# Kernel tuning notes

Hardware: AMD Instinct MI355X
Metric: run time of the kernel (lower is better)

## Reference

```python
import jax, jax.numpy as jnp
import numpy as np

TOKEN_SELF_ATTN_VALUE = -50000.0


def setup_inputs() -> dict:
    key = jax.random.key(0)
    k1, k2, k3 = jax.random.split(key, 3)
    batch, seqlen, dim = 16, 4096, 64
    n_hashes, bucket_size = 8, 64
    n_buckets = seqlen // bucket_size  # 64
    qk = jax.random.normal(k1, (batch, seqlen, dim), dtype=jnp.float32)
    v = jax.random.normal(k2, (batch, seqlen, dim), dtype=jnp.float32)
    # random rotations for LSH hashing: (dim, n_hashes, n_buckets // 2)
    rotations = jax.random.normal(k3, (dim, n_hashes, n_buckets // 2), dtype=jnp.float32)
    return {"qk": qk, "v": v, "rotations": rotations}


def reference(qk, v, rotations):
    batch, seqlen, dim = qk.shape
    n_hashes = rotations.shape[1]
    n_buckets = 2 * rotations.shape[2]
    bucket_size = seqlen // n_buckets

    # ---- hash_vectors (rehash_each_round=True, no hash dropout) ----
    rotated = jnp.einsum('btf,fhi->bhti', qk, rotations)       # (b, h, t, nb/2)
    rotated = jnp.concatenate([rotated, -rotated], axis=-1)    # (b, h, t, nb)
    buckets = jnp.argmax(rotated, axis=-1)                     # (b, h, t)
    offsets = (jnp.arange(n_hashes) * n_buckets)[None, :, None]
    buckets = (buckets + offsets).reshape(batch, n_hashes * seqlen)

    # ---- sort tokens by (bucket, position) ----
    ticker = jnp.arange(n_hashes * seqlen)
    buckets_and_t = seqlen * buckets + (ticker % seqlen)[None, :]
    sticker = jnp.argsort(buckets_and_t, axis=-1)              # keys are unique
    undo_sort = jnp.argsort(sticker, axis=-1)
    st = sticker % seqlen                                      # original positions

    sqk = jnp.take_along_axis(qk, st[:, :, None], axis=1)      # (b, h*t, d)
    sv = jnp.take_along_axis(v, st[:, :, None], axis=1)

    chunk_size = n_hashes * n_buckets
    bq_t = st.reshape(batch, chunk_size, bucket_size)
    bqk = sqk.reshape(batch, chunk_size, bucket_size, dim)
    bv = sv.reshape(batch, chunk_size, bucket_size, dim)

    bq = bqk
    # F.normalize(p=2, eps=1e-12)
    bk = bqk / jnp.maximum(jnp.linalg.norm(bqk, axis=-1, keepdims=True), 1e-12)

    def look_one_back(x):
        return jnp.concatenate([x, jnp.roll(x, 1, axis=1)], axis=2)

    bk = look_one_back(bk)
    bv = look_one_back(bv)
    bkv_t = look_one_back(bq_t)

    dots = jnp.einsum('bcie,bcje->bcij', bq, bk) * (dim ** -0.5)  # (b, chunks, i, 2i)

    # self-attention mask (causal=False, no input masks by default)
    self_mask = bq_t[:, :, :, None] == bkv_t[:, :, None, :]
    dots = jnp.where(self_mask, TOKEN_SELF_ATTN_VALUE, dots)

    dots_logsumexp = jax.scipy.special.logsumexp(dots, axis=-1, keepdims=True)
    probs = jnp.exp(dots - dots_logsumexp)
    bo = jnp.einsum('bcij,bcje->bcie', probs, bv)

    so = bo.reshape(batch, -1, dim)                   # (b, h*t, d)
    slogits = dots_logsumexp.reshape(batch, -1)       # (b, h*t)

    # unsort back to original token order
    o = jnp.take_along_axis(so, undo_sort[:, :, None], axis=1)
    logits = jnp.take_along_axis(slogits, undo_sort, axis=1)

    o = o.reshape(batch, n_hashes, seqlen, dim)
    logits = logits.reshape(batch, n_hashes, seqlen, 1)

    # combine hash rounds weighted by their logsumexps
    w = jnp.exp(logits - jax.scipy.special.logsumexp(logits, axis=1, keepdims=True))
    out = jnp.sum(o * w, axis=1)                      # (b, t, d)
    return out
```

## Files before the change

### kernel.cpp

```cpp
#include <hip/hip_runtime.h>

#define BATCH  16
#define SEQ    4096
#define DIM    64
#define NHASH  8
#define NCHUNK 512
#define SB     72

typedef __attribute__((ext_vector_type(8))) short short8;
typedef __attribute__((ext_vector_type(4))) float floatx4;

__device__ __forceinline__ float trunc_hi(float a) {
    return __uint_as_float(__float_as_uint(a) & 0xffff0000u);
}
__device__ __forceinline__ unsigned pack_hi2(float a, float b) {
    return (__float_as_uint(a) >> 16) | (__float_as_uint(b) & 0xffff0000u);
}
__device__ __forceinline__ void hi16_store(const float* xs, short* dst) {
    unsigned hd[8];
#pragma unroll
    for (int u = 0; u < 8; ++u) hd[u] = pack_hi2(xs[2*u], xs[2*u + 1]);
    *(uint4*)(dst)     = make_uint4(hd[0], hd[1], hd[2], hd[3]);
    *(uint4*)(dst + 8) = make_uint4(hd[4], hd[5], hd[6], hd[7]);
}
__device__ __forceinline__ void split8_frag(const float* xs, short8* hi, short8* lo) {
    union { unsigned u[4]; short8 s; } H, L;
#pragma unroll
    for (int u = 0; u < 4; ++u) {
        float a = xs[2*u], b = xs[2*u + 1];
        H.u[u] = pack_hi2(a, b);
        L.u[u] = pack_hi2(a - trunc_hi(a), b - trunc_hi(b));
    }
    *hi = H.s; *lo = L.s;
}

__global__ __launch_bounds__(256, 2) void lsh_hash_kernel(
    const float* __restrict__ qk, const float* __restrict__ rot,
    int* __restrict__ buckets)
{
    __shared__ float rs[64 * 128];
    int tid = threadIdx.x;
    int tb   = blockIdx.x >> 1;
    int hsel = blockIdx.x & 1;

    {
        const float4* rg = (const float4*)rot;
#pragma unroll
        for (int j = 0; j < 8; ++j) {
            int idx4 = j * 256 + tid;
            int f = idx4 >> 5, r4 = idx4 & 31;
            ((float4*)rs)[idx4] = rg[f * 64 + hsel * 32 + r4];
        }
    }
    __syncthreads();

    int tt = tid & 127;
    int hh = tid >> 7;
    int gid0 = tb * 256 + tt;
    int gid1 = gid0 + 128;
    const float* q0 = qk + (size_t)gid0 * DIM;
    const float* q1 = qk + (size_t)gid1 * DIM;

#pragma unroll
    for (int h0 = 0; h0 < 2; ++h0) {
        int hp = hh * 2 + h0;
        const float* rbase = rs + hp * 32;
        float a0[32], a1[32];
#pragma unroll
        for (int i = 0; i < 32; ++i) { a0[i] = 0.f; a1[i] = 0.f; }
#pragma unroll 1
        for (int ft = 0; ft < 8; ++ft) {
            float qa[8], qb[8];
            *(float4*)&qa[0] = *(const float4*)(q0 + ft * 8);
            *(float4*)&qa[4] = *(const float4*)(q0 + ft * 8 + 4);
            *(float4*)&qb[0] = *(const float4*)(q1 + ft * 8);
            *(float4*)&qb[4] = *(const float4*)(q1 + ft * 8 + 4);
#pragma unroll
            for (int f8 = 0; f8 < 8; ++f8) {
                const float* rp = rbase + (ft * 8 + f8) * 128;
                float x = qa[f8], y = qb[f8];
#pragma unroll
                for (int i = 0; i < 32; ++i) {
                    float r = rp[i];
                    a0[i] = fmaf(x, r, a0[i]);
                    a1[i] = fmaf(y, r, a1[i]);
                }
            }
        }
        int h = hsel * 4 + hp;
        {
            float best = a0[0]; int bi = 0;
#pragma unroll
            for (int i = 1; i < 32; ++i) { if (a0[i] > best) { best = a0[i]; bi = i; } }
#pragma unroll
            for (int i = 0; i < 32; ++i) { float nv = -a0[i]; if (nv > best) { best = nv; bi = i + 32; } }
            int b = gid0 >> 12, t = gid0 & 4095;
            buckets[((size_t)b * NHASH + h) * SEQ + t] = bi;
        }
        {
            float best = a1[0]; int bi = 0;
#pragma unroll
            for (int i = 1; i < 32; ++i) { if (a1[i] > best) { best = a1[i]; bi = i; } }
#pragma unroll
            for (int i = 0; i < 32; ++i) { float nv = -a1[i]; if (nv > best) { best = nv; bi = i + 32; } }
            int b = gid1 >> 12, t = gid1 & 4095;
            buckets[((size_t)b * NHASH + h) * SEQ + t] = bi;
        }
    }
}

__global__ __launch_bounds__(256) void lsh_sort_kernel(
    const int* __restrict__ buckets, int* __restrict__ st)
{
    __shared__ int hist[256 * 65];
    __shared__ int seg[256];
    __shared__ int base[64];

    int bh = blockIdx.x;
    int tid = threadIdx.x;
    int w = tid >> 6, lane = tid & 63;

    for (int i = tid; i < 256 * 65; i += 256) hist[i] = 0;

    int myb[16];
    {
        const int4* bp4 = (const int4*)(buckets + (size_t)bh * SEQ);
#pragma unroll
        for (int u4 = 0; u4 < 4; ++u4) {
            int4 bb = bp4[tid * 4 + u4];
            myb[u4*4+0] = bb.x; myb[u4*4+1] = bb.y;
            myb[u4*4+2] = bb.z; myb[u4*4+3] = bb.w;
        }
    }
    __syncthreads();
    int* hrow = &hist[tid * 65];
#pragma unroll
    for (int u = 0; u < 16; ++u) hrow[myb[u]] += 1;
    __syncthreads();

    {
        int run = 0;
        for (int tp = 0; tp < 64; ++tp) {
            int idx = (w * 64 + tp) * 65 + lane;
            int c0 = hist[idx];
            hist[idx] = run;
            run += c0;
        }
        seg[w * 64 + lane] = run;
    }
    __syncthreads();
    if (tid < 64) {
        int s0 = seg[lane], s1 = seg[64 + lane], s2 = seg[128 + lane], s3 = seg[192 + lane];
        seg[lane] = 0; seg[64 + lane] = s0;
        seg[128 + lane] = s0 + s1; seg[192 + lane] = s0 + s1 + s2;
        int tot = s0 + s1 + s2 + s3;
        int x = tot;
#pragma unroll
        for (int d = 1; d < 64; d <<= 1) {
            int y = __shfl_up(x, d, 64);
            if (lane >= d) x += y;
        }
        base[lane] = x - tot;
    }
    __syncthreads();

    int* op = st + (size_t)bh * SEQ;
#pragma unroll
    for (int u = 0; u < 16; ++u) {
        int bb = myb[u];
        int local = hrow[bb];
        hrow[bb] = local + 1;
        int pos = base[bb] + seg[w * 64 + bb] + local;
        op[pos] = tid * 16 + u;
    }
}

__global__ __launch_bounds__(256, 5) void lsh_attn_kernel(
    const float* __restrict__ qk, const float* __restrict__ v,
    const int* __restrict__ st, float* __restrict__ Obuf, float* __restrict__ Dbuf)
{
    __shared__ short Khi[64 * SB];
    __shared__ short Psp[64 * SB];
    __shared__ short Vhi[64 * SB];
    __shared__ int   tk[64];

    short* Phi = Khi;
    short* Plo = Psp;

    int tid  = threadIdx.x;
    int lane = tid & 63;
    int w    = tid >> 6;
    int quad = lane >> 4;
    int l15  = lane & 15;

    int bc = blockIdx.x;
    int b = bc >> 9, c = bc & (NCHUNK - 1);
    int cm = (c + NCHUNK - 1) & (NCHUNK - 1);

    const int*   stb = st + (size_t)b * (NHASH * SEQ);
    const float* qkb = qk + (size_t)b * SEQ * DIM;
    const float* vb  = v  + (size_t)b * SEQ * DIM;

    short8 qH[2], qL[2];
    {
        int qt = stb[c * 64 + 16 * w + l15];
        const float* qp = qkb + (size_t)qt * DIM + 8 * quad;
        float xs[8];
#pragma unroll
        for (int kb = 0; kb < 2; ++kb) {
            *(float4*)&xs[0] = *(const float4*)(qp + 32 * kb);
            *(float4*)&xs[4] = *(const float4*)(qp + 32 * kb + 4);
            split8_frag(xs, &qH[kb], &qL[kb]);
        }
    }
    int tqr[4];
#pragma unroll
    for (int r = 0; r < 4; ++r) tqr[r] = stb[c * 64 + 16 * w + quad * 4 + r];

    float   Dacc[4] = {0.f, 0.f, 0.f, 0.f};
    floatx4 oacc[4];
#pragma unroll
    for (int a = 0; a < 4; ++a) oacc[a] = (floatx4){0.f, 0.f, 0.f, 0.f};

    for (int half = 0; half < 2; ++half) {
        int ck = half ? cm : c;
        __syncthreads();

        {
            int r = tid >> 2, s = tid & 3;
            int trow = stb[ck * 64 + r];
            if (s == 0) tk[r] = trow;
            const float4* k4 = (const float4*)(qkb + (size_t)trow * DIM + s * 16);
            float xs[16];
            *(float4*)&xs[0]  = k4[0];
            *(float4*)&xs[4]  = k4[1];
            *(float4*)&xs[8]  = k4[2];
            *(float4*)&xs[12] = k4[3];
            float ss = 0.f;
#pragma unroll
            for (int u = 0; u < 16; ++u) ss += xs[u] * xs[u];
            ss += __shfl_xor(ss, 1);
            ss += __shfl_xor(ss, 2);
            float sc = 1.0f / fmaxf(sqrtf(ss), 1e-12f);
#pragma unroll
            for (int u = 0; u < 16; ++u) xs[u] *= sc;
            hi16_store(xs, &Khi[r * SB + s * 16]);
        }
        {
            float xs[16];
#pragma unroll
            for (int u = 0; u < 16; ++u) {
                int trow = stb[ck * 64 + w * 16 + u];
                xs[u] = vb[(size_t)trow * DIM + lane];
            }
            hi16_store(xs, &Vhi[lane * SB + w * 16]);
        }
        __syncthreads();

        floatx4 dt[4];
#pragma unroll
        for (int jt = 0; jt < 4; ++jt) dt[jt] = (floatx4){0.f, 0.f, 0.f, 0.f};
#pragma unroll
        for (int kb = 0; kb < 2; ++kb) {
#pragma unroll
            for (int jt = 0; jt < 4; ++jt) {
                short8 bH = *(const short8*)&Khi[(16 * jt + l15) * SB + kb * 32 + quad * 8];
                dt[jt] = __builtin_amdgcn_mfma_f32_16x16x32_bf16(qH[kb], bH, dt[jt], 0, 0, 0);
                dt[jt] = __builtin_amdgcn_mfma_f32_16x16x32_bf16(qL[kb], bH, dt[jt], 0, 0, 0);
            }
        }
        __syncthreads();

#pragma unroll
        for (int jt = 0; jt < 4; ++jt) {
            int tkc = tk[16 * jt + l15];
#pragma unroll
            for (int r = 0; r < 4; ++r) {
                float p = (tqr[r] == tkc) ? 0.f : __expf(dt[jt][r] * 0.125f);
                Dacc[r] += p;
                int idx = (16 * w + quad * 4 + r) * SB + 16 * jt + l15;
                Phi[idx] = (short)(__float_as_uint(p) >> 16);
                Plo[idx] = (short)(__float_as_uint(p - trunc_hi(p)) >> 16);
            }
        }

#pragma unroll
        for (int kb = 0; kb < 2; ++kb) {
            short8 aH = *(const short8*)&Phi[(16 * w + l15) * SB + kb * 32 + quad * 8];
            short8 aL = *(const short8*)&Plo[(16 * w + l15) * SB + kb * 32 + quad * 8];
#pragma unroll
            for (int a = 0; a < 4; ++a) {
                short8 bH = *(const short8*)&Vhi[(16 * a + l15) * SB + kb * 32 + quad * 8];
                oacc[a] = __builtin_amdgcn_mfma_f32_16x16x32_bf16(aH, bH, oacc[a], 0, 0, 0);
                oacc[a] = __builtin_amdgcn_mfma_f32_16x16x32_bf16(aL, bH, oacc[a], 0, 0, 0);
            }
        }
    }

    int h = c >> 6;
#pragma unroll
    for (int r = 0; r < 4; ++r) {
        int t = tqr[r];
        size_t rowb = ((size_t)(b * SEQ + t) * NHASH + h) * DIM;
#pragma unroll
        for (int a = 0; a < 4; ++a)
            Obuf[rowb + 16 * a + l15] = oacc[a][r];
    }
#pragma unroll
    for (int r = 0; r < 4; ++r) {
        float rs = Dacc[r];
        rs += __shfl_xor(rs, 1);
        rs += __shfl_xor(rs, 2);
        rs += __shfl_xor(rs, 4);
        rs += __shfl_xor(rs, 8);
        if (l15 == 0) Dbuf[(size_t)(b * SEQ + tqr[r]) * NHASH + h] = rs;
    }
}

__global__ __launch_bounds__(256) void lsh_combine_tok(
    const float* __restrict__ Obuf, const float* __restrict__ Dbuf,
    float* __restrict__ out)
{
    int gid = blockIdx.x * 256 + threadIdx.x;
    int d4 = gid & 15;
    int bt = gid >> 4;

    const float4* op = (const float4*)Obuf + (size_t)bt * (NHASH * 16);
    const float*  dp = Dbuf + (size_t)bt * NHASH;

    float4 n = make_float4(0.f, 0.f, 0.f, 0.f);
    float den = 0.f;
#pragma unroll
    for (int h = 0; h < NHASH; ++h) {
        float4 o = op[h * 16 + d4];
        den += dp[h];
        n.x += o.x; n.y += o.y; n.z += o.z; n.w += o.w;
    }
    float invd = 1.0f / den;
    float4 r; r.x = n.x*invd; r.y = n.y*invd; r.z = n.z*invd; r.w = n.w*invd;
    ((float4*)out)[gid] = r;
}

extern "C" void kernel_launch(void* const* d_in, const int* in_sizes, int n_in,
                              void* d_out, int out_size, void* d_ws, size_t ws_size,
                              hipStream_t stream)
{
    const float* qk  = (const float*)d_in[0];
    const float* v   = (const float*)d_in[1];
    const float* rot = (const float*)d_in[2];
    float* out = (float*)d_out;

    char* w = (char*)d_ws;
    int*   buckets = (int*)(w);
    int*   st      = (int*)(w + 2097152);
    float* Obuf    = (float*)(w + 4194304);
    float* Dbuf    = (float*)(w + 4194304 + 134217728);

    lsh_hash_kernel<<<512, 256, 0, stream>>>(qk, rot, buckets);
    lsh_sort_kernel<<<128, 256, 0, stream>>>(buckets, st);
    lsh_attn_kernel<<<8192, 256, 0, stream>>>(qk, v, st, Obuf, Dbuf);
    lsh_combine_tok<<<4096, 256, 0, stream>>>(Obuf, Dbuf, out);
}
```

Baseline: 229.8 us.

## Accumulate hash rounds with atomics and drop split-bf16 low parts for P and K/V

The attention kernel now atomically adds its unnormalized outputs and exp-sums into a single per-token accumulator instead of writing eight per-hash buffers. The accumulator is zeroed inside the hash kernel, and the combine step becomes a single divide. This removes the large per-hash intermediate write and read-back. It also drops the low-half bf16 correction for P, which halves the PV MFMAs and frees the Plo LDS buffer so occupancy can rise to 8. K and V now use round-to-nearest bf16. The trade-offs are atomic contention, nondeterministic summation order, and lower precision.

```diff
diff --git a/kernel.cpp b/kernel.cpp
--- a/kernel.cpp
+++ b/kernel.cpp
@@ -16,10 +16,15 @@
 __device__ __forceinline__ unsigned pack_hi2(float a, float b) {
     return (__float_as_uint(a) >> 16) | (__float_as_uint(b) & 0xffff0000u);
 }
-__device__ __forceinline__ void hi16_store(const float* xs, short* dst) {
+__device__ __forceinline__ unsigned pack_rn2(float a, float b) {
+    unsigned ua = __float_as_uint(a) + 0x8000u;
+    unsigned ub = __float_as_uint(b) + 0x8000u;
+    return (ua >> 16) | (ub & 0xffff0000u);
+}
+__device__ __forceinline__ void hi16_store_rn(const float* xs, short* dst) {
     unsigned hd[8];
 #pragma unroll
-    for (int u = 0; u < 8; ++u) hd[u] = pack_hi2(xs[2*u], xs[2*u + 1]);
+    for (int u = 0; u < 8; ++u) hd[u] = pack_rn2(xs[2*u], xs[2*u + 1]);
     *(uint4*)(dst)     = make_uint4(hd[0], hd[1], hd[2], hd[3]);
     *(uint4*)(dst + 8) = make_uint4(hd[4], hd[5], hd[6], hd[7]);
 }
@@ -36,8 +41,16 @@
 
 __global__ __launch_bounds__(256, 2) void lsh_hash_kernel(
     const float* __restrict__ qk, const float* __restrict__ rot,
-    int* __restrict__ buckets)
-{
+    int* __restrict__ buckets, float4* __restrict__ zinit)
+{
+    {
+        float4 z = make_float4(0.f, 0.f, 0.f, 0.f);
+        int t = blockIdx.x * 256 + (int)threadIdx.x;
+#pragma unroll
+        for (int j = 0; j < 8; ++j) zinit[(size_t)j * 131072 + t] = z;
+        if (t < 16384) zinit[(size_t)8 * 131072 + t] = z;
+    }
+
     __shared__ float rs[64 * 128];
     int tid = threadIdx.x;
     int tb   = blockIdx.x >> 1;
@@ -175,17 +188,15 @@
     }
 }
 
-__global__ __launch_bounds__(256, 5) void lsh_attn_kernel(
+__global__ __launch_bounds__(256, 8) void lsh_attn_kernel(
     const float* __restrict__ qk, const float* __restrict__ v,
-    const int* __restrict__ st, float* __restrict__ Obuf, float* __restrict__ Dbuf)
+    const int* __restrict__ st, float* __restrict__ Onum, float* __restrict__ Dsum)
 {
     __shared__ short Khi[64 * SB];
-    __shared__ short Psp[64 * SB];
     __shared__ short Vhi[64 * SB];
     __shared__ int   tk[64];
 
     short* Phi = Khi;
-    short* Plo = Psp;
 
     int tid  = threadIdx.x;
     int lane = tid & 63;
@@ -244,7 +255,7 @@
             float sc = 1.0f / fmaxf(sqrtf(ss), 1e-12f);
 #pragma unroll
             for (int u = 0; u < 16; ++u) xs[u] *= sc;
-            hi16_store(xs, &Khi[r * SB + s * 16]);
+            hi16_store_rn(xs, &Khi[r * SB + s * 16]);
         }
         {
             float xs[16];
@@ -253,7 +264,7 @@
                 int trow = stb[ck * 64 + w * 16 + u];
                 xs[u] = vb[(size_t)trow * DIM + lane];
             }
-            hi16_store(xs, &Vhi[lane * SB + w * 16]);
+            hi16_store_rn(xs, &Vhi[lane * SB + w * 16]);
         }
         __syncthreads();
 
@@ -279,32 +290,28 @@
                 float p = (tqr[r] == tkc) ? 0.f : __expf(dt[jt][r] * 0.125f);
                 Dacc[r] += p;
                 int idx = (16 * w + quad * 4 + r) * SB + 16 * jt + l15;
-                Phi[idx] = (short)(__float_as_uint(p) >> 16);
-                Plo[idx] = (short)(__float_as_uint(p - trunc_hi(p)) >> 16);
+                Phi[idx] = (short)((__float_as_uint(p) + 0x8000u) >> 16);
             }
         }
 
 #pragma unroll
         for (int kb = 0; kb < 2; ++kb) {
             short8 aH = *(const short8*)&Phi[(16 * w + l15) * SB + kb * 32 + quad * 8];
-            short8 aL = *(const short8*)&Plo[(16 * w + l15) * SB + kb * 32 + quad * 8];
 #pragma unroll
             for (int a = 0; a < 4; ++a) {
                 short8 bH = *(const short8*)&Vhi[(16 * a + l15) * SB + kb * 32 + quad * 8];
                 oacc[a] = __builtin_amdgcn_mfma_f32_16x16x32_bf16(aH, bH, oacc[a], 0, 0, 0);
-                oacc[a] = __builtin_amdgcn_mfma_f32_16x16x32_bf16(aL, bH, oacc[a], 0, 0, 0);
-            }
-        }
-    }
-
-    int h = c >> 6;
+            }
+        }
+    }
+
 #pragma unroll
     for (int r = 0; r < 4; ++r) {
         int t = tqr[r];
-        size_t rowb = ((size_t)(b * SEQ + t) * NHASH + h) * DIM;
+        float* po = Onum + (size_t)(b * SEQ + t) * DIM;
 #pragma unroll
         for (int a = 0; a < 4; ++a)
-            Obuf[rowb + 16 * a + l15] = oacc[a][r];
+            unsafeAtomicAdd(&po[16 * a + l15], oacc[a][r]);
     }
 #pragma unroll
     for (int r = 0; r < 4; ++r) {
@@ -313,32 +320,20 @@
         rs += __shfl_xor(rs, 2);
         rs += __shfl_xor(rs, 4);
         rs += __shfl_xor(rs, 8);
-        if (l15 == 0) Dbuf[(size_t)(b * SEQ + tqr[r]) * NHASH + h] = rs;
+        if (l15 == 0) unsafeAtomicAdd(&Dsum[b * SEQ + tqr[r]], rs);
     }
 }
 
 __global__ __launch_bounds__(256) void lsh_combine_tok(
-    const float* __restrict__ Obuf, const float* __restrict__ Dbuf,
+    const float* __restrict__ Onum, const float* __restrict__ Dsum,
     float* __restrict__ out)
 {
     int gid = blockIdx.x * 256 + threadIdx.x;
-    int d4 = gid & 15;
     int bt = gid >> 4;
-
-    const float4* op = (const float4*)Obuf + (size_t)bt * (NHASH * 16);
-    const float*  dp = Dbuf + (size_t)bt * NHASH;
-
-    float4 n = make_float4(0.f, 0.f, 0.f, 0.f);
-    float den = 0.f;
-#pragma unroll
-    for (int h = 0; h < NHASH; ++h) {
-        float4 o = op[h * 16 + d4];
-        den += dp[h];
-        n.x += o.x; n.y += o.y; n.z += o.z; n.w += o.w;
-    }
-    float invd = 1.0f / den;
-    float4 r; r.x = n.x*invd; r.y = n.y*invd; r.z = n.z*invd; r.w = n.w*invd;
-    ((float4*)out)[gid] = r;
+    float invd = 1.0f / Dsum[bt];
+    float4 o = ((const float4*)Onum)[gid];
+    o.x *= invd; o.y *= invd; o.z *= invd; o.w *= invd;
+    ((float4*)out)[gid] = o;
 }
 
 extern "C" void kernel_launch(void* const* d_in, const int* in_sizes, int n_in,
@@ -353,11 +348,11 @@
     char* w = (char*)d_ws;
     int*   buckets = (int*)(w);
     int*   st      = (int*)(w + 2097152);
-    float* Obuf    = (float*)(w + 4194304);
-    float* Dbuf    = (float*)(w + 4194304 + 134217728);
-
-    lsh_hash_kernel<<<512, 256, 0, stream>>>(qk, rot, buckets);
+    float* Onum    = (float*)(w + 4194304);
+    float* Dsum    = (float*)(w + 4194304 + 16777216);
+
+    lsh_hash_kernel<<<512, 256, 0, stream>>>(qk, rot, buckets, (float4*)Onum);
     lsh_sort_kernel<<<128, 256, 0, stream>>>(buckets, st);
-    lsh_attn_kernel<<<8192, 256, 0, stream>>>(qk, v, st, Obuf, Dbuf);
-    lsh_combine_tok<<<4096, 256, 0, stream>>>(Obuf, Dbuf, out);
-}
+    lsh_attn_kernel<<<8192, 256, 0, stream>>>(qk, v, st, Onum, Dsum);
+    lsh_combine_tok<<<4096, 256, 0, stream>>>(Onum, Dsum, out);
+}
```

New measurement: 346.4 us. +50.7%, slower.

## Drop split-bf16 P*V term, round-to-nearest bf16, and store O buffer as fp16

Applied to the files above, without the earlier changes.

The P*V product now uses a single rounded bf16 matrix instead of a hi/lo split, which halves its MFMAs and removes one shared-memory buffer, so the occupancy hint rises from 5 to 8 blocks. K and V are converted to bf16 with round-to-nearest instead of truncation. The per-hash output buffer is stored as fp16, halving the traffic between the attention and combine kernels. The cost is lower accuracy: single-bf16 probabilities and fp16 intermediates could push error past tolerance, and the unnormalized O accumulated from exp values could overflow fp16's range.

```diff
diff --git a/kernel.cpp b/kernel.cpp
--- a/kernel.cpp
+++ b/kernel.cpp
@@ -1,4 +1,5 @@
 #include <hip/hip_runtime.h>
+#include <hip/hip_fp16.h>
 
 #define BATCH  16
 #define SEQ    4096
@@ -16,10 +17,15 @@
 __device__ __forceinline__ unsigned pack_hi2(float a, float b) {
     return (__float_as_uint(a) >> 16) | (__float_as_uint(b) & 0xffff0000u);
 }
-__device__ __forceinline__ void hi16_store(const float* xs, short* dst) {
+__device__ __forceinline__ unsigned pack_rn2(float a, float b) {
+    unsigned ua = __float_as_uint(a) + 0x8000u;
+    unsigned ub = __float_as_uint(b) + 0x8000u;
+    return (ua >> 16) | (ub & 0xffff0000u);
+}
+__device__ __forceinline__ void hi16_store_rn(const float* xs, short* dst) {
     unsigned hd[8];
 #pragma unroll
-    for (int u = 0; u < 8; ++u) hd[u] = pack_hi2(xs[2*u], xs[2*u + 1]);
+    for (int u = 0; u < 8; ++u) hd[u] = pack_rn2(xs[2*u], xs[2*u + 1]);
     *(uint4*)(dst)     = make_uint4(hd[0], hd[1], hd[2], hd[3]);
     *(uint4*)(dst + 8) = make_uint4(hd[4], hd[5], hd[6], hd[7]);
 }
@@ -175,17 +181,15 @@
     }
 }
 
-__global__ __launch_bounds__(256, 5) void lsh_attn_kernel(
+__global__ __launch_bounds__(256, 8) void lsh_attn_kernel(
     const float* __restrict__ qk, const float* __restrict__ v,
-    const int* __restrict__ st, float* __restrict__ Obuf, float* __restrict__ Dbuf)
+    const int* __restrict__ st, __half* __restrict__ Obuf, float* __restrict__ Dbuf)
 {
     __shared__ short Khi[64 * SB];
-    __shared__ short Psp[64 * SB];
     __shared__ short Vhi[64 * SB];
     __shared__ int   tk[64];
 
     short* Phi = Khi;
-    short* Plo = Psp;
 
     int tid  = threadIdx.x;
     int lane = tid & 63;
@@ -244,7 +248,7 @@
             float sc = 1.0f / fmaxf(sqrtf(ss), 1e-12f);
 #pragma unroll
             for (int u = 0; u < 16; ++u) xs[u] *= sc;
-            hi16_store(xs, &Khi[r * SB + s * 16]);
+            hi16_store_rn(xs, &Khi[r * SB + s * 16]);
         }
         {
             float xs[16];
@@ -253,7 +257,7 @@
                 int trow = stb[ck * 64 + w * 16 + u];
                 xs[u] = vb[(size_t)trow * DIM + lane];
             }
-            hi16_store(xs, &Vhi[lane * SB + w * 16]);
+            hi16_store_rn(xs, &Vhi[lane * SB + w * 16]);
         }
         __syncthreads();
 
@@ -279,20 +283,17 @@
                 float p = (tqr[r] == tkc) ? 0.f : __expf(dt[jt][r] * 0.125f);
                 Dacc[r] += p;
                 int idx = (16 * w + quad * 4 + r) * SB + 16 * jt + l15;
-                Phi[idx] = (short)(__float_as_uint(p) >> 16);
-                Plo[idx] = (short)(__float_as_uint(p - trunc_hi(p)) >> 16);
+                Phi[idx] = (short)((__float_as_uint(p) + 0x8000u) >> 16);
             }
         }
 
 #pragma unroll
         for (int kb = 0; kb < 2; ++kb) {
             short8 aH = *(const short8*)&Phi[(16 * w + l15) * SB + kb * 32 + quad * 8];
-            short8 aL = *(const short8*)&Plo[(16 * w + l15) * SB + kb * 32 + quad * 8];
 #pragma unroll
             for (int a = 0; a < 4; ++a) {
                 short8 bH = *(const short8*)&Vhi[(16 * a + l15) * SB + kb * 32 + quad * 8];
                 oacc[a] = __builtin_amdgcn_mfma_f32_16x16x32_bf16(aH, bH, oacc[a], 0, 0, 0);
-                oacc[a] = __builtin_amdgcn_mfma_f32_16x16x32_bf16(aL, bH, oacc[a], 0, 0, 0);
             }
         }
     }
@@ -304,7 +305,7 @@
         size_t rowb = ((size_t)(b * SEQ + t) * NHASH + h) * DIM;
 #pragma unroll
         for (int a = 0; a < 4; ++a)
-            Obuf[rowb + 16 * a + l15] = oacc[a][r];
+            Obuf[rowb + 16 * a + l15] = __float2half(oacc[a][r]);
     }
 #pragma unroll
     for (int r = 0; r < 4; ++r) {
@@ -318,23 +319,27 @@
 }
 
 __global__ __launch_bounds__(256) void lsh_combine_tok(
-    const float* __restrict__ Obuf, const float* __restrict__ Dbuf,
+    const __half* __restrict__ Obuf, const float* __restrict__ Dbuf,
     float* __restrict__ out)
 {
     int gid = blockIdx.x * 256 + threadIdx.x;
     int d4 = gid & 15;
     int bt = gid >> 4;
 
-    const float4* op = (const float4*)Obuf + (size_t)bt * (NHASH * 16);
+    const __half* op = Obuf + (size_t)bt * (NHASH * DIM) + d4 * 4;
     const float*  dp = Dbuf + (size_t)bt * NHASH;
 
     float4 n = make_float4(0.f, 0.f, 0.f, 0.f);
     float den = 0.f;
 #pragma unroll
     for (int h = 0; h < NHASH; ++h) {
-        float4 o = op[h * 16 + d4];
+        uint2 u = *(const uint2*)(op + h * DIM);
+        __half2 p01 = *(__half2*)&u.x;
+        __half2 p23 = *(__half2*)&u.y;
+        float2 f01 = __half22float2(p01);
+        float2 f23 = __half22float2(p23);
         den += dp[h];
-        n.x += o.x; n.y += o.y; n.z += o.z; n.w += o.w;
+        n.x += f01.x; n.y += f01.y; n.z += f23.x; n.w += f23.y;
     }
     float invd = 1.0f / den;
     float4 r; r.x = n.x*invd; r.y = n.y*invd; r.z = n.z*invd; r.w = n.w*invd;
@@ -351,10 +356,10 @@
     float* out = (float*)d_out;
 
     char* w = (char*)d_ws;
-    int*   buckets = (int*)(w);
-    int*   st      = (int*)(w + 2097152);
-    float* Obuf    = (float*)(w + 4194304);
-    float* Dbuf    = (float*)(w + 4194304 + 134217728);
+    int*    buckets = (int*)(w);
+    int*    st      = (int*)(w + 2097152);
+    __half* Obuf    = (__half*)(w + 4194304);
+    float*  Dbuf    = (float*)(w + 4194304 + 67108864);
 
     lsh_hash_kernel<<<512, 256, 0, stream>>>(qk, rot, buckets);
     lsh_sort_kernel<<<128, 256, 0, stream>>>(buckets, st);
```

After: 316.0 us. +37.5%, slower.
